# Kernel optimization log

Hardware: AMD Instinct MI355X
Metric: run time of the kernel (lower is better)

The kernel has to match this reference:

```python
import jax, jax.numpy as jnp
import numpy as np

B, C, N, K_NN = 16, 64, 2048, 3
OUT_C = 64


def setup_inputs() -> dict:
    key = jax.random.key(0)
    k1, k2, k3 = jax.random.split(key, 3)
    x = jax.random.normal(k1, (B, C, N), dtype=jnp.float32)
    fan_in = C * K_NN
    bound = 1.0 / np.sqrt(fan_in)
    W = jax.random.uniform(k2, (OUT_C, C, K_NN), minval=-bound, maxval=bound, dtype=jnp.float32)
    b = jax.random.uniform(k3, (OUT_C,), minval=-bound, maxval=bound, dtype=jnp.float32)
    return {"x": x, "W": W, "b": b}


def reference(x, W, b):
    # x: [B, C, N]; W: [O, C, K]; b: [O]
    K = W.shape[-1]
    # Pairwise squared distances: dist[b,i,j] = |x_i|^2 + |x_j|^2 - 2 x_i.x_j.
    # The original takes sqrt, but sqrt is monotone and the distances are only
    # used for top-k index selection, so we select on squared distances (same indices).
    norm_sq = jnp.sum(x * x, axis=1)                      # [B, N]
    dot = jnp.einsum('bcn,bcm->bnm', x, x)                # [B, N, N]
    dist_sq = norm_sq[:, :, None] + norm_sq[:, None, :] - 2.0 * dot  # [B, N, N]
    # K smallest distances per row -> neighbor indices [B, N, K]
    _, idx = jax.lax.top_k(-dist_sq, K)
    # Gather neighbors: neigh[b, c, n, k] = x[b, c, idx[b, n, k]]
    neigh = jax.vmap(lambda xb, ib: xb[:, ib])(x, idx)    # [B, C, N, K]
    # Conv1d with kernel_size == stride == K over the flattened [B, C, N*K]
    # tensor is exactly a per-window contraction over the K neighbors.
    out = jnp.einsum('bcnk,ock->bon', neigh, W) + b[None, :, None]  # [B, O, N]
    return out
```

## Files before the change

kernel.cpp:

```cpp
#include <hip/hip_runtime.h>
#include <cfloat>
#include <climits>

#define B_DIM 16
#define C_DIM 64
#define N_DIM 2048
#define O_DIM 64
#define K_NN  3

typedef __attribute__((ext_vector_type(8))) short bf16x8;
typedef __attribute__((ext_vector_type(4))) float floatx4;

__device__ __forceinline__ unsigned short f32_to_bf16_rne(float f) {
  unsigned int u = __float_as_uint(f);
  return (unsigned short)((u + 0x7fffu + ((u >> 16) & 1u)) >> 16);
}
__device__ __forceinline__ float bf16_to_f32(unsigned short h) {
  return __uint_as_float(((unsigned int)h) << 16);
}

__device__ __forceinline__ void insert3d(double d, int j,
    double &k0, double &k1, double &k2, int &j0, int &j1, int &j2) {
  bool c2 = (d < k2) || (d == k2 && j < j2);
  bool c1 = (d < k1) || (d == k1 && j < j1);
  bool c0 = (d < k0) || (d == k0 && j < j0);
  k2 = c1 ? k1 : (c2 ? d : k2);
  j2 = c1 ? j1 : (c2 ? j : j2);
  k1 = c0 ? k0 : (c1 ? d : k1);
  j1 = c0 ? j0 : (c1 ? j : j1);
  k0 = c0 ? d : k0;
  j0 = c0 ? j : j0;
}

__device__ __forceinline__ void ins4(float key, int jv, float* k, int* j) {
  bool c3 = key < k[3], c2 = key < k[2], c1 = key < k[1], c0 = key < k[0];
  k[3] = c2 ? k[2] : (c3 ? key : k[3]);
  j[3] = c2 ? j[2] : (c3 ? jv  : j[3]);
  k[2] = c1 ? k[1] : (c2 ? key : k[2]);
  j[2] = c1 ? j[1] : (c2 ? jv  : j[2]);
  k[1] = c0 ? k[0] : (c1 ? key : k[1]);
  j[1] = c0 ? j[0] : (c1 ? jv  : j[1]);
  k[0] = c0 ? key : k[0];
  j[0] = c0 ? jv  : j[0];
}

__global__ __launch_bounds__(256) void prep_kernel(
    const float* __restrict__ x, float* __restrict__ xT,
    unsigned short* __restrict__ xTh, unsigned short* __restrict__ xTl,
    double* __restrict__ nd, float* __restrict__ nf) {
  __shared__ __align__(16) float xs[C_DIM][68];
  int bid = blockIdx.x;
  int b  = bid >> 5;
  int n0 = (bid & 31) * 64;
  int t = threadIdx.x;
  const float* xb = x + (size_t)b * C_DIM * N_DIM;
  #pragma unroll
  for (int r = 0; r < 4; ++r) {
    int idx = r * 256 + t;
    int c = idx >> 4;
    int qq = idx & 15;
    *(float4*)&xs[c][qq * 4] = *(const float4*)(xb + (size_t)c * N_DIM + n0 + qq * 4);
  }
  __syncthreads();
  int n = t >> 2, cg = t & 3;
  float v[16];
  #pragma unroll
  for (int cc = 0; cc < 16; ++cc) v[cc] = xs[cg * 16 + cc][n];
  double ps = 0.0;
  #pragma unroll
  for (int cc = 0; cc < 16; ++cc) ps = fma((double)v[cc], (double)v[cc], ps);
  ps += __shfl_xor(ps, 1, 64);
  ps += __shfl_xor(ps, 2, 64);
  size_t row = (size_t)b * N_DIM + n0 + n;
  #pragma unroll
  for (int qq = 0; qq < 4; ++qq) {
    float4 wv; wv.x = v[qq*4]; wv.y = v[qq*4+1]; wv.z = v[qq*4+2]; wv.w = v[qq*4+3];
    *(float4*)&xT[row * C_DIM + cg * 16 + qq * 4] = wv;
  }
  unsigned short hh[16], ll[16];
  #pragma unroll
  for (int cc = 0; cc < 16; ++cc) {
    hh[cc] = f32_to_bf16_rne(v[cc]);
    ll[cc] = f32_to_bf16_rne(v[cc] - bf16_to_f32(hh[cc]));
  }
  #pragma unroll
  for (int e = 0; e < 2; ++e) {
    int phys = (2 * cg + e) ^ (n & 7);
    unsigned int hp[4], lp[4];
    #pragma unroll
    for (int xk = 0; xk < 4; ++xk) {
      hp[xk] = (unsigned)hh[e*8 + 2*xk] | ((unsigned)hh[e*8 + 2*xk + 1] << 16);
      lp[xk] = (unsigned)ll[e*8 + 2*xk] | ((unsigned)ll[e*8 + 2*xk + 1] << 16);
    }
    ((uint4*)xTh)[row * 8 + phys] = *(uint4*)hp;
    ((uint4*)xTl)[row * 8 + phys] = *(uint4*)lp;
  }
  if (cg == 0) {
    nd[row] = ps;
    nf[row] = (float)ps;
  }
}

__global__ __launch_bounds__(256) void wt_kernel(const float* __restrict__ W,
                                                 float* __restrict__ Wt) {
  int t = blockIdx.x * 256 + threadIdx.x;
  int o  = t / (C_DIM * K_NN);
  int ck = t - o * (C_DIM * K_NN);
  Wt[ck * O_DIM + o] = W[t];
}

__global__ __launch_bounds__(256, 4) void topk_kernel(
    const unsigned short* __restrict__ xTh, const unsigned short* __restrict__ xTl,
    const float* __restrict__ nf, int* __restrict__ cand) {
  __shared__ __align__(16) unsigned short Jh[128 * 64];
  __shared__ __align__(16) unsigned short Jl[128 * 64];
  int bid   = blockIdx.x;
  int q     = bid & 3;
  int itile = (bid >> 2) & 31;
  int b     = bid >> 7;
  int i0    = itile * 64;
  int jq0   = q * 512;
  int t = threadIdx.x;
  int w = t >> 6, lane = t & 63, quad = lane >> 4, col = lane & 15;
  int csw = col & 7;
  const unsigned short* xh = xTh + (size_t)b * N_DIM * 64;
  const unsigned short* xl = xTl + (size_t)b * N_DIM * 64;
  const float* nfb = nf + b * N_DIM;

  bf16x8 ih[2], il[2];
  #pragma unroll
  for (int ks = 0; ks < 2; ++ks) {
    size_t row = i0 + w * 16 + col;
    int phys = (ks * 4 + quad) ^ csw;
    ih[ks] = *(const bf16x8*)(xh + row * 64 + phys * 8);
    il[ks] = *(const bf16x8*)(xl + row * 64 + phys * 8);
  }

  float ck[4]; int cj[4];
  #pragma unroll
  for (int s = 0; s < 4; ++s) { ck[s] = FLT_MAX; cj[s] = 0; }

  int a0 = col * 64 + ((quad ^ csw) * 8);
  int a1 = col * 64 + (((4 + quad) ^ csw) * 8);

  for (int js = 0; js < 4; ++js) {
    int j0 = jq0 + js * 128;
    __syncthreads();
    {
      const unsigned short* sh = xh + (size_t)(j0 + w * 32) * 64;
      const unsigned short* sl = xl + (size_t)(j0 + w * 32) * 64;
      unsigned short* dh = &Jh[w * 32 * 64];
      unsigned short* dl = &Jl[w * 32 * 64];
      int off = lane * 8;
      #pragma unroll
      for (int k2 = 0; k2 < 4; ++k2) {
        *(uint4*)(dh + k2 * 512 + off) = *(const uint4*)(sh + k2 * 512 + off);
        *(uint4*)(dl + k2 * 512 + off) = *(const uint4*)(sl + k2 * 512 + off);
      }
    }
    __syncthreads();

    floatx4 acc[8];
    #pragma unroll
    for (int jt = 0; jt < 8; ++jt) acc[jt] = (floatx4){0.f, 0.f, 0.f, 0.f};

    #pragma unroll
    for (int ks = 0; ks < 2; ++ks) {
      int ab = ks ? a1 : a0;
      #pragma unroll
      for (int jt = 0; jt < 8; ++jt) {
        bf16x8 jh = *(const bf16x8*)&Jh[jt * 1024 + ab];
        bf16x8 jl = *(const bf16x8*)&Jl[jt * 1024 + ab];
        acc[jt] = __builtin_amdgcn_mfma_f32_16x16x32_bf16(jl, ih[ks], acc[jt], 0, 0, 0);
        acc[jt] = __builtin_amdgcn_mfma_f32_16x16x32_bf16(jh, il[ks], acc[jt], 0, 0, 0);
        acc[jt] = __builtin_amdgcn_mfma_f32_16x16x32_bf16(jh, ih[ks], acc[jt], 0, 0, 0);
      }
    }

    int jb = j0 + quad * 4;
    #pragma unroll
    for (int jt = 0; jt < 8; ++jt) {
      float4 nv = *(const float4*)(nfb + jb + jt * 16);
      float nfa[4] = {nv.x, nv.y, nv.z, nv.w};
      #pragma unroll
      for (int r = 0; r < 4; ++r) {
        float key = fmaf(-2.0f, acc[jt][r], nfa[r]);
        int jv = jb + jt * 16 + r;
        ins4(key, jv, ck, cj);
      }
    }
  }

  #pragma unroll
  for (int m = 16; m < 64; m <<= 1) {
    float tk[4]; int tj[4];
    #pragma unroll
    for (int s = 0; s < 4; ++s) {
      tk[s] = __shfl_xor(ck[s], m, 64);
      tj[s] = __shfl_xor(cj[s], m, 64);
    }
    #pragma unroll
    for (int s = 0; s < 4; ++s) ins4(tk[s], tj[s], ck, cj);
  }
  if (quad == 0) {
    int row = b * N_DIM + i0 + w * 16 + col;
    int base = row * 16 + q * 4;
    #pragma unroll
    for (int s = 0; s < 4; ++s) cand[base + s] = cj[s];
  }
}

__global__ __launch_bounds__(256) void refine_kernel(
    const float* __restrict__ xT, const double* __restrict__ nd,
    const int* __restrict__ cand, int* __restrict__ topk) {
  int t = threadIdx.x;
  int lane = t & 63;
  int row = blockIdx.x * 4 + (t >> 6);
  int b = row >> 11;
  int n = row & (N_DIM - 1);
  int cid = lane >> 2;
  int seg = lane & 3;
  int j = cand[row * 16 + cid];
  const float* xn = xT + (((size_t)b * N_DIM + n) * C_DIM) + seg * 16;
  const float* xj = xT + (((size_t)b * N_DIM + j) * C_DIM) + seg * 16;
  double dot = 0.0;
  #pragma unroll
  for (int qq = 0; qq < 4; ++qq) {
    float4 a  = *(const float4*)(xn + qq * 4);
    float4 bb = *(const float4*)(xj + qq * 4);
    dot = fma((double)a.x, (double)bb.x, dot);
    dot = fma((double)a.y, (double)bb.y, dot);
    dot = fma((double)a.z, (double)bb.z, dot);
    dot = fma((double)a.w, (double)bb.w, dot);
  }
  dot += __shfl_xor(dot, 1, 64);
  dot += __shfl_xor(dot, 2, 64);
  double key = fma(-2.0, dot, nd[b * N_DIM + j]);
  double k0 = key, k1 = DBL_MAX, k2 = DBL_MAX;
  int j0 = j, j1 = INT_MAX, j2 = INT_MAX;
  #pragma unroll
  for (int m = 4; m < 64; m <<= 1) {
    double t0 = __shfl_xor(k0, m, 64);
    double t1 = __shfl_xor(k1, m, 64);
    double t2 = __shfl_xor(k2, m, 64);
    int    u0 = __shfl_xor(j0, m, 64);
    int    u1 = __shfl_xor(j1, m, 64);
    int    u2 = __shfl_xor(j2, m, 64);
    insert3d(t0, u0, k0, k1, k2, j0, j1, j2);
    insert3d(t1, u1, k0, k1, k2, j0, j1, j2);
    insert3d(t2, u2, k0, k1, k2, j0, j1, j2);
  }
  if (lane == 0) {
    int base = row * K_NN;
    topk[base + 0] = j0;
    topk[base + 1] = j1;
    topk[base + 2] = j2;
  }
}

#define NT   64
#define NPAD 68
__global__ __launch_bounds__(256) void conv_kernel(
    const float* __restrict__ xT, const float* __restrict__ Wt,
    const float* __restrict__ bias, const int* __restrict__ topk,
    float* __restrict__ out) {
  __shared__ __align__(16) float nb[C_DIM * K_NN][NPAD];
  int bid = blockIdx.x;
  int b  = bid >> 5;
  int n0 = (bid & 31) * NT;
  const float* xtb = xT + (size_t)b * N_DIM * C_DIM;
  const int* tk = topk + (b * N_DIM + n0) * K_NN;
  int t = threadIdx.x;

  #pragma unroll
  for (int p = 0; p < 12; ++p) {
    int u = p * 256 + t;
    int seg = u & 15;
    int r   = u >> 4;
    int k = r >> 6, n = r & 63;
    int j = tk[n * K_NN + k];
    float4 v = *(const float4*)(xtb + (size_t)j * C_DIM + seg * 4);
    nb[(seg * 4 + 0) * 3 + k][n] = v.x;
    nb[(seg * 4 + 1) * 3 + k][n] = v.y;
    nb[(seg * 4 + 2) * 3 + k][n] = v.z;
    nb[(seg * 4 + 3) * 3 + k][n] = v.w;
  }
  __syncthreads();

  int ng = t & 15, og = t >> 4;
  float acc[4][4];
  #pragma unroll
  for (int oo = 0; oo < 4; ++oo) {
    float bv = bias[(og << 2) + oo];
    #pragma unroll
    for (int nn = 0; nn < 4; ++nn) acc[oo][nn] = bv;
  }
  const float* nbp = &nb[0][0] + (ng << 2);
  const float* wtp = Wt + (og << 2);
  #pragma unroll 4
  for (int ckk = 0; ckk < C_DIM * K_NN; ++ckk) {
    float4 nv = *(const float4*)(nbp + ckk * NPAD);
    float4 wv = *(const float4*)(wtp + ckk * O_DIM);
    float na[4] = {nv.x, nv.y, nv.z, nv.w};
    float wa[4] = {wv.x, wv.y, wv.z, wv.w};
    #pragma unroll
    for (int oo = 0; oo < 4; ++oo)
      #pragma unroll
      for (int nn = 0; nn < 4; ++nn)
        acc[oo][nn] = fmaf(wa[oo], na[nn], acc[oo][nn]);
  }
  #pragma unroll
  for (int oo = 0; oo < 4; ++oo) {
    int o = (og << 2) + oo;
    float4 v; v.x = acc[oo][0]; v.y = acc[oo][1]; v.z = acc[oo][2]; v.w = acc[oo][3];
    *(float4*)&out[(size_t)(b * O_DIM + o) * N_DIM + n0 + (ng << 2)] = v;
  }
}

extern "C" void kernel_launch(void* const* d_in, const int* in_sizes, int n_in,
                              void* d_out, int out_size, void* d_ws, size_t ws_size,
                              hipStream_t stream) {
  const float* x    = (const float*)d_in[0];
  const float* W    = (const float*)d_in[1];
  const float* bias = (const float*)d_in[2];
  float* out = (float*)d_out;
  char* ws = (char*)d_ws;
  float*          xT  = (float*)ws;
  unsigned short* xTh = (unsigned short*)(ws + 8388608);
  unsigned short* xTl = (unsigned short*)(ws + 12582912);
  double*         nd  = (double*)(ws + 16777216);
  float*          nfp = (float*)(ws + 17039360);
  int*            cd  = (int*)(ws + 17170432);
  int*            tk  = (int*)(ws + 19267584);
  float*          Wt  = (float*)(ws + 19660800);

  prep_kernel<<<B_DIM * (N_DIM / 64), 256, 0, stream>>>(x, xT, xTh, xTl, nd, nfp);
  wt_kernel<<<(O_DIM * C_DIM * K_NN) / 256, 256, 0, stream>>>(W, Wt);
  topk_kernel<<<B_DIM * 32 * 4, 256, 0, stream>>>(xTh, xTl, nfp, cd);
  refine_kernel<<<(B_DIM * N_DIM) / 4, 256, 0, stream>>>(xT, nd, cd, tk);
  conv_kernel<<<B_DIM * (N_DIM / NT), 256, 0, stream>>>(xT, Wt, bias, tk, out);
}
```

Before: 166.1 us.

## Fold weight transpose into prep kernel and use packed-key min-reduction in refine

The standalone weight-transpose kernel is merged into the prep kernel as 48 extra blocks, which removes one kernel launch. The refine kernel's shuffle-based 3-way sorted merge over doubles is replaced by packing the distance and the index into one 64-bit key and running three min-reductions. The key now adds both norms plus 1.0 so it stays positive and integer comparison orders it correctly, but the low 11 mantissa bits are truncated, which could change tie handling. The topk kernel's launch-bounds occupancy hint is also raised from 4 to 5 waves.

New measurement: 169.9 us. 2.3% more time.

```diff
diff --git a/kernel.cpp b/kernel.cpp
--- a/kernel.cpp
+++ b/kernel.cpp
@@ -17,19 +17,6 @@
 }
 __device__ __forceinline__ float bf16_to_f32(unsigned short h) {
   return __uint_as_float(((unsigned int)h) << 16);
-}
-
-__device__ __forceinline__ void insert3d(double d, int j,
-    double &k0, double &k1, double &k2, int &j0, int &j1, int &j2) {
-  bool c2 = (d < k2) || (d == k2 && j < j2);
-  bool c1 = (d < k1) || (d == k1 && j < j1);
-  bool c0 = (d < k0) || (d == k0 && j < j0);
-  k2 = c1 ? k1 : (c2 ? d : k2);
-  j2 = c1 ? j1 : (c2 ? j : j2);
-  k1 = c0 ? k0 : (c1 ? d : k1);
-  j1 = c0 ? j0 : (c1 ? j : j1);
-  k0 = c0 ? d : k0;
-  j0 = c0 ? j : j0;
 }
 
 __device__ __forceinline__ void ins4(float key, int jv, float* k, int* j) {
@@ -47,12 +34,20 @@
 __global__ __launch_bounds__(256) void prep_kernel(
     const float* __restrict__ x, float* __restrict__ xT,
     unsigned short* __restrict__ xTh, unsigned short* __restrict__ xTl,
-    double* __restrict__ nd, float* __restrict__ nf) {
+    double* __restrict__ nd, float* __restrict__ nf,
+    const float* __restrict__ W, float* __restrict__ Wt) {
+  int bid = blockIdx.x;
+  int t = threadIdx.x;
+  if (bid >= 512) {
+    int t2 = (bid - 512) * 256 + t;
+    int o  = t2 / (C_DIM * K_NN);
+    int ck = t2 - o * (C_DIM * K_NN);
+    Wt[ck * O_DIM + o] = W[t2];
+    return;
+  }
   __shared__ __align__(16) float xs[C_DIM][68];
-  int bid = blockIdx.x;
   int b  = bid >> 5;
   int n0 = (bid & 31) * 64;
-  int t = threadIdx.x;
   const float* xb = x + (size_t)b * C_DIM * N_DIM;
   #pragma unroll
   for (int r = 0; r < 4; ++r) {
@@ -101,15 +96,7 @@
   }
 }
 
-__global__ __launch_bounds__(256) void wt_kernel(const float* __restrict__ W,
-                                                 float* __restrict__ Wt) {
-  int t = blockIdx.x * 256 + threadIdx.x;
-  int o  = t / (C_DIM * K_NN);
-  int ck = t - o * (C_DIM * K_NN);
-  Wt[ck * O_DIM + o] = W[t];
-}
-
-__global__ __launch_bounds__(256, 4) void topk_kernel(
+__global__ __launch_bounds__(256, 5) void topk_kernel(
     const unsigned short* __restrict__ xTh, const unsigned short* __restrict__ xTl,
     const float* __restrict__ nf, int* __restrict__ cand) {
   __shared__ __align__(16) unsigned short Jh[128 * 64];
@@ -235,26 +222,28 @@
   }
   dot += __shfl_xor(dot, 1, 64);
   dot += __shfl_xor(dot, 2, 64);
-  double key = fma(-2.0, dot, nd[b * N_DIM + j]);
-  double k0 = key, k1 = DBL_MAX, k2 = DBL_MAX;
-  int j0 = j, j1 = INT_MAX, j2 = INT_MAX;
-  #pragma unroll
-  for (int m = 4; m < 64; m <<= 1) {
-    double t0 = __shfl_xor(k0, m, 64);
-    double t1 = __shfl_xor(k1, m, 64);
-    double t2 = __shfl_xor(k2, m, 64);
-    int    u0 = __shfl_xor(j0, m, 64);
-    int    u1 = __shfl_xor(j1, m, 64);
-    int    u2 = __shfl_xor(j2, m, 64);
-    insert3d(t0, u0, k0, k1, k2, j0, j1, j2);
-    insert3d(t1, u1, k0, k1, k2, j0, j1, j2);
-    insert3d(t2, u2, k0, k1, k2, j0, j1, j2);
+  double key = fma(-2.0, dot, nd[b * N_DIM + j] + nd[b * N_DIM + n]) + 1.0;
+  unsigned long long u =
+      ((unsigned long long)__double_as_longlong(key) & ~2047ull) |
+      (unsigned long long)(unsigned)j;
+  unsigned long long v = u;
+  int jout[3];
+  #pragma unroll
+  for (int p = 0; p < 3; ++p) {
+    unsigned long long m = v;
+    #pragma unroll
+    for (int msk = 4; msk < 64; msk <<= 1) {
+      unsigned long long o = __shfl_xor(m, msk, 64);
+      m = (o < m) ? o : m;
+    }
+    jout[p] = (int)(m & 2047ull);
+    v = (v == m) ? ~0ull : v;
   }
   if (lane == 0) {
     int base = row * K_NN;
-    topk[base + 0] = j0;
-    topk[base + 1] = j1;
-    topk[base + 2] = j2;
+    topk[base + 0] = jout[0];
+    topk[base + 1] = jout[1];
+    topk[base + 2] = jout[2];
   }
 }
 
@@ -334,8 +323,7 @@
   int*            tk  = (int*)(ws + 19267584);
   float*          Wt  = (float*)(ws + 19660800);
 
-  prep_kernel<<<B_DIM * (N_DIM / 64), 256, 0, stream>>>(x, xT, xTh, xTl, nd, nfp);
-  wt_kernel<<<(O_DIM * C_DIM * K_NN) / 256, 256, 0, stream>>>(W, Wt);
+  prep_kernel<<<512 + 48, 256, 0, stream>>>(x, xT, xTh, xTl, nd, nfp, W, Wt);
   topk_kernel<<<B_DIM * 32 * 4, 256, 0, stream>>>(xTh, xTl, nfp, cd);
   refine_kernel<<<(B_DIM * N_DIM) / 4, 256, 0, stream>>>(xT, nd, cd, tk);
   conv_kernel<<<B_DIM * (N_DIM / NT), 256, 0, stream>>>(xT, Wt, bias, tk, out);
```
